# Optimization experiments

Measured on AMD Instinct MI355X. Metric: run time of the kernel, lower is better.

Reference implementation:

```python
import jax, jax.numpy as jnp
import numpy as np

N_REQ = 100000
N_CODE = 100000
C_IN = 256
C_OUT = 256
HEADS = 8
DIM = C_OUT // HEADS  # 32
E = 500000
E_LAB = 200000
NEG_SLOPE = 0.2
BN_EPS = 1e-5


def setup_inputs() -> dict:
    key = jax.random.key(0)
    ks = jax.random.split(key, 20)
    s = 0.05
    return {
        "x_req": jax.random.normal(ks[0], (N_REQ, C_IN), jnp.float32),
        "x_code": jax.random.normal(ks[1], (N_CODE, C_IN), jnp.float32),
        "edge_index_rc": jax.random.randint(ks[2], (2, E), 0, N_CODE),  # req -> code
        "edge_index_cr": jax.random.randint(ks[3], (2, E), 0, N_REQ),   # code -> req
        "edge_label_index": jax.random.randint(ks[4], (2, E_LAB), 0, N_REQ),
        # per-node-type projections
        "W_req": jax.random.normal(ks[5], (C_OUT, C_IN), jnp.float32) * s,
        "b_req": jnp.zeros((C_OUT,), jnp.float32),
        "W_code": jax.random.normal(ks[6], (C_OUT, C_IN), jnp.float32) * s,
        "b_code": jnp.zeros((C_OUT,), jnp.float32),
        # per-edge-type attention vectors [heads, dim]
        "att_src_rc": jax.random.normal(ks[7], (HEADS, DIM), jnp.float32) * s,
        "att_dst_rc": jax.random.normal(ks[8], (HEADS, DIM), jnp.float32) * s,
        "att_src_cr": jax.random.normal(ks[9], (HEADS, DIM), jnp.float32) * s,
        "att_dst_cr": jax.random.normal(ks[10], (HEADS, DIM), jnp.float32) * s,
        # semantic-level attention
        "k_W": jax.random.normal(ks[11], (C_OUT, C_OUT), jnp.float32) * s,
        "k_b": jnp.zeros((C_OUT,), jnp.float32),
        "q": jax.random.normal(ks[12], (C_OUT,), jnp.float32) * s,
        # BatchNorm1d affine params (shared bn1 applied to each node type)
        "gamma": jnp.ones((C_OUT,), jnp.float32),
        "beta": jnp.zeros((C_OUT,), jnp.float32),
    }


def _segment_softmax(logits, seg, num_segments):
    # logits: [E, H], softmax over edges sharing the same destination node
    m = jax.ops.segment_max(logits, seg, num_segments=num_segments)
    m = jnp.where(jnp.isfinite(m), m, 0.0)
    e = jnp.exp(logits - m[seg])
    s = jax.ops.segment_sum(e, seg, num_segments=num_segments)
    return e / (s[seg] + 1e-16)


def _han_edge(x_src, x_dst, edge_index, att_s, att_d, n_dst):
    # x_src: [N_src, H, D], x_dst: [N_dst, H, D]
    a_s = jnp.einsum('nhd,hd->nh', x_src, att_s)
    a_d = jnp.einsum('nhd,hd->nh', x_dst, att_d)
    src, dst = edge_index[0], edge_index[1]
    alpha = jax.nn.leaky_relu(a_s[src] + a_d[dst], NEG_SLOPE)   # [E, H]
    alpha = _segment_softmax(alpha, dst, n_dst)
    msg = x_src[src] * alpha[:, :, None]                        # [E, H, D]
    out = jax.ops.segment_sum(msg, dst, num_segments=n_dst)     # [N_dst, H, D]
    return jax.nn.relu(out.reshape(n_dst, HEADS * DIM))


def _group(outs, q, k_W, k_b):
    # semantic-level attention over metapaths (PyG HANConv group)
    stacked = jnp.stack(outs)                                   # [M, N, C]
    k = jnp.tanh(stacked @ k_W.T + k_b).mean(axis=1)            # [M, C]
    attn = jax.nn.softmax((q * k).sum(-1))                      # [M]
    return jnp.einsum('m,mnc->nc', attn, stacked)


def _batchnorm(x, gamma, beta):
    mu = x.mean(axis=0)
    var = x.var(axis=0)  # biased, as torch BN uses for normalization
    return (x - mu) * jax.lax.rsqrt(var + BN_EPS) * gamma + beta


def reference(x_req, x_code, edge_index_rc, edge_index_cr, edge_label_index,
              W_req, b_req, W_code, b_code,
              att_src_rc, att_dst_rc, att_src_cr, att_dst_cr,
              k_W, k_b, q, gamma, beta):
    # node-type projections -> [N, H, D]
    h_req = (x_req @ W_req.T + b_req).reshape(-1, HEADS, DIM)
    h_code = (x_code @ W_code.T + b_code).reshape(-1, HEADS, DIM)

    # per-edge-type GAT-style propagation
    out_code = _han_edge(h_req, h_code, edge_index_rc, att_src_rc, att_dst_rc, N_CODE)
    out_req = _han_edge(h_code, h_req, edge_index_cr, att_src_cr, att_dst_cr, N_REQ)

    # semantic attention fusion (one metapath per node type here)
    z_req = _group([out_req], q, k_W, k_b)
    z_code = _group([out_code], q, k_W, k_b)

    # shared BatchNorm1d applied per node type (training-mode batch stats)
    z_req = _batchnorm(z_req, gamma, beta)
    z_code = _batchnorm(z_code, gamma, beta)

    # edge dot-product classifier
    feat_req = z_req[edge_label_index[0]]
    feat_code = z_code[edge_label_index[1]]
    return jax.nn.sigmoid((feat_req * feat_code).sum(axis=-1))
```

## Files before the change

kernel.cpp:

```cpp
#include <hip/hip_runtime.h>
#include <cstdint>
#include <cstddef>

namespace {

constexpr int kN    = 100000;
constexpr int kNpad = 100096;
constexpr int kE    = 500000;
constexpr int kEL   = 200000;
constexpr int kC    = 256;
constexpr int kH    = 8;
constexpr float kNegSlope = 0.2f;
constexpr float kBnEps    = 1e-5f;

typedef float    f32x4  __attribute__((ext_vector_type(4)));
typedef __bf16   bf16x8 __attribute__((ext_vector_type(8)));
typedef _Float16 h4     __attribute__((ext_vector_type(4)));

__device__ inline unsigned short bf16_rtn(float x) {
  unsigned u = __builtin_bit_cast(unsigned, x);
  unsigned r = (u + 0x7fffu + ((u >> 16) & 1u)) >> 16;
  return (unsigned short)r;
}
__device__ inline float bf16_f(unsigned short h) {
  unsigned u = ((unsigned)h) << 16;
  return __builtin_bit_cast(float, u);
}

__device__ inline void async_copy16(unsigned short* lds, const unsigned short* g) {
  __builtin_amdgcn_global_load_lds(
      (const __attribute__((address_space(1))) unsigned int*)g,
      (__attribute__((address_space(3))) unsigned int*)lds, 16, 0, 0);
}

__global__ void zero_kernel(int* __restrict__ p, int n) {
  const int i = blockIdx.x * 256 + threadIdx.x;
  if (i < n) p[i] = 0;
}

__global__ __launch_bounds__(256) void cvt_kernel(
    const float* __restrict__ in, unsigned short* __restrict__ hi,
    unsigned short* __restrict__ lo, int n4) {
  const int i = blockIdx.x * 256 + threadIdx.x;
  if (i >= n4) return;
  const float4 v = ((const float4*)in)[i];
  const unsigned short h0 = bf16_rtn(v.x), h1 = bf16_rtn(v.y),
                       h2 = bf16_rtn(v.z), h3 = bf16_rtn(v.w);
  ((ushort4*)hi)[i] = make_ushort4(h0, h1, h2, h3);
  ((ushort4*)lo)[i] = make_ushort4(bf16_rtn(v.x - bf16_f(h0)),
                                   bf16_rtn(v.y - bf16_f(h1)),
                                   bf16_rtn(v.z - bf16_f(h2)),
                                   bf16_rtn(v.w - bf16_f(h3)));
}

__global__ __launch_bounds__(256) void gemm_kernel(
    const unsigned short* __restrict__ Ahi, const unsigned short* __restrict__ Alo,
    const unsigned short* __restrict__ Bhi, const unsigned short* __restrict__ Blo,
    const float* __restrict__ bias, _Float16* __restrict__ H, int M) {
  __shared__ unsigned short sAhi[128 * 32];
  __shared__ unsigned short sAlo[128 * 32];
  __shared__ unsigned short sBhi[128 * 32];
  __shared__ unsigned short sBlo[128 * 32];

  const int tid  = threadIdx.x;
  const int m0   = blockIdx.y * 128;
  const int n0   = blockIdx.x * 128;
  const int w    = tid >> 6, lane = tid & 63, l16 = lane & 15, quad = lane >> 4;
  const int wm   = (w >> 1) * 64, wn = (w & 1) * 64;

  const unsigned short* gsrc = (w == 0) ? Ahi : (w == 1) ? Alo : (w == 2) ? Bhi : Blo;
  unsigned short* lds        = (w == 0) ? sAhi : (w == 1) ? sAlo : (w == 2) ? sBhi : sBlo;
  const int row0 = (w < 2) ? m0 : n0;
  const size_t gbase = (size_t)(row0 + (lane >> 2)) * kC + (lane & 3) * 8;

  f32x4 acc[4][4] = {};

  for (int kt = 0; kt < kC / 32; ++kt) {
    const int k0 = kt * 32;
    __syncthreads();
#pragma unroll
    for (int j = 0; j < 8; ++j)
      async_copy16(lds + j * 512, gsrc + gbase + (size_t)j * 16 * kC + k0);
    __syncthreads();

    bf16x8 ah[4], al[4], bh[4], bl[4];
#pragma unroll
    for (int mi = 0; mi < 4; ++mi) {
      const int row = wm + mi * 16 + l16;
      ah[mi] = *(const bf16x8*)&sAhi[row * 32 + quad * 8];
      al[mi] = *(const bf16x8*)&sAlo[row * 32 + quad * 8];
    }
#pragma unroll
    for (int ni = 0; ni < 4; ++ni) {
      const int row = wn + ni * 16 + l16;
      bh[ni] = *(const bf16x8*)&sBhi[row * 32 + quad * 8];
      bl[ni] = *(const bf16x8*)&sBlo[row * 32 + quad * 8];
    }
#pragma unroll
    for (int mi = 0; mi < 4; ++mi)
#pragma unroll
      for (int ni = 0; ni < 4; ++ni) {
        acc[mi][ni] = __builtin_amdgcn_mfma_f32_16x16x32_bf16(ah[mi], bh[ni], acc[mi][ni], 0, 0, 0);
        acc[mi][ni] = __builtin_amdgcn_mfma_f32_16x16x32_bf16(ah[mi], bl[ni], acc[mi][ni], 0, 0, 0);
        acc[mi][ni] = __builtin_amdgcn_mfma_f32_16x16x32_bf16(al[mi], bh[ni], acc[mi][ni], 0, 0, 0);
      }
  }

#pragma unroll
  for (int ni = 0; ni < 4; ++ni) {
    const int col = n0 + wn + ni * 16 + l16;
    const float bc = bias[col];
#pragma unroll
    for (int mi = 0; mi < 4; ++mi) {
      const int gm0 = m0 + wm + mi * 16 + quad * 4;
#pragma unroll
      for (int r = 0; r < 4; ++r) {
        const int gm = gm0 + r;
        if (gm < M) H[(size_t)gm * kC + col] = (_Float16)(acc[mi][ni][r] + bc);
      }
    }
  }
}

__global__ __launch_bounds__(256) void avec_kernel(
    const _Float16* __restrict__ h, const float* __restrict__ attA,
    const float* __restrict__ attB, float* __restrict__ outA,
    float* __restrict__ outB, int N) {
  const int n = blockIdx.x * 4 + (threadIdx.x >> 6);
  if (n >= N) return;
  const int L = threadIdx.x & 63;
  const h4 hv = *(const h4*)&h[(size_t)n * kC + 4 * L];
  const float4 a = *(const float4*)&attA[4 * L];
  const float4 b = *(const float4*)&attB[4 * L];
  const float hx = (float)hv.x, hy = (float)hv.y, hz = (float)hv.z, hw = (float)hv.w;
  float pa = hx * a.x + hy * a.y + hz * a.z + hw * a.w;
  float pb = hx * b.x + hy * b.y + hz * b.z + hw * b.w;
  for (int m = 1; m < 8; m <<= 1) {
    pa += __shfl_xor(pa, m);
    pb += __shfl_xor(pb, m);
  }
  if ((L & 7) == 0) {
    outA[n * kH + (L >> 3)] = pa;
    outB[n * kH + (L >> 3)] = pb;
  }
}

__global__ void count_kernel(const int* __restrict__ dst, int E, int* __restrict__ cnt) {
  const int e = blockIdx.x * 256 + threadIdx.x;
  if (e < E) atomicAdd(&cnt[dst[e]], 1);
}

__global__ void scan1_kernel(const int* __restrict__ cnt, int N,
                             int* __restrict__ off, int* __restrict__ part) {
  __shared__ int s[256];
  const int t = threadIdx.x;
  const int i = blockIdx.x * 256 + t;
  const int v = (i < N) ? cnt[i] : 0;
  s[t] = v;
  __syncthreads();
  for (int o = 1; o < 256; o <<= 1) {
    const int x = (t >= o) ? s[t - o] : 0;
    __syncthreads();
    s[t] += x;
    __syncthreads();
  }
  if (i < N) off[i] = s[t] - v;
  if (t == 255) part[blockIdx.x] = s[255];
}

__global__ void scan2_kernel(int* __restrict__ part, int NB) {
  __shared__ int s[512];
  const int t = threadIdx.x;
  const int v = (t < NB) ? part[t] : 0;
  s[t] = v;
  __syncthreads();
  for (int o = 1; o < 512; o <<= 1) {
    const int x = (t >= o) ? s[t - o] : 0;
    __syncthreads();
    s[t] += x;
    __syncthreads();
  }
  if (t < NB) part[t] = s[t] - v;
}

__global__ void scan3_kernel(int* __restrict__ off, int* __restrict__ cur,
                             const int* __restrict__ part, int N) {
  const int i = blockIdx.x * 256 + threadIdx.x;
  if (i < N) {
    const int v = off[i] + part[blockIdx.x];
    off[i] = v;
    cur[i] = v;
  }
}

__global__ void scatter_kernel(const int* __restrict__ dst,
                               const int* __restrict__ srcv, int E,
                               int* __restrict__ cur, int* __restrict__ perm) {
  const int e = blockIdx.x * 256 + threadIdx.x;
  if (e < E) {
    const int p = atomicAdd(&cur[dst[e]], 1);
    perm[p] = srcv[e];
  }
}

__global__ __launch_bounds__(256) void aggregate2_kernel(
    const _Float16* __restrict__ h0, const float* __restrict__ aS0,
    const float* __restrict__ aD0, const int* __restrict__ srcs0,
    const int* __restrict__ off0, const int* __restrict__ cnt0,
    float* __restrict__ out0,
    const _Float16* __restrict__ h1, const float* __restrict__ aS1,
    const float* __restrict__ aD1, const int* __restrict__ srcs1,
    const int* __restrict__ off1, const int* __restrict__ cnt1,
    float* __restrict__ out1) {
  const int d = blockIdx.x * 4 + (threadIdx.x >> 6);
  if (d >= kN) return;
  const bool dir1 = (blockIdx.y != 0);
  const _Float16* __restrict__ hsrc = dir1 ? h1 : h0;
  const float* __restrict__ aS   = dir1 ? aS1 : aS0;
  const float* __restrict__ aD   = dir1 ? aD1 : aD0;
  const int* __restrict__ srcs   = dir1 ? srcs1 : srcs0;
  const int* __restrict__ off    = dir1 ? off1 : off0;
  const int* __restrict__ cnt    = dir1 ? cnt1 : cnt0;
  float* __restrict__ out        = dir1 ? out1 : out0;

  const int L  = threadIdx.x & 63;
  const int hd = L >> 3;
  const float ad = aD[d * kH + hd];
  const int o = off[d], c = cnt[d];
  float4 acc = make_float4(0.f, 0.f, 0.f, 0.f);
  float se = 0.f;
  int i = 0;
  for (; i + 4 <= c; i += 4) {
    const int s0 = srcs[o + i], s1 = srcs[o + i + 1];
    const int s2 = srcs[o + i + 2], s3 = srcs[o + i + 3];
    const float a0 = aS[s0 * kH + hd], a1 = aS[s1 * kH + hd];
    const float a2 = aS[s2 * kH + hd], a3 = aS[s3 * kH + hd];
    const h4 v0 = *(const h4*)&hsrc[(size_t)s0 * kC + 4 * L];
    const h4 v1 = *(const h4*)&hsrc[(size_t)s1 * kC + 4 * L];
    const h4 v2 = *(const h4*)&hsrc[(size_t)s2 * kC + 4 * L];
    const h4 v3 = *(const h4*)&hsrc[(size_t)s3 * kC + 4 * L];
    float t0 = a0 + ad; t0 = t0 > 0.f ? t0 : kNegSlope * t0;
    float t1 = a1 + ad; t1 = t1 > 0.f ? t1 : kNegSlope * t1;
    float t2 = a2 + ad; t2 = t2 > 0.f ? t2 : kNegSlope * t2;
    float t3 = a3 + ad; t3 = t3 > 0.f ? t3 : kNegSlope * t3;
    const float w0 = __expf(t0), w1 = __expf(t1);
    const float w2 = __expf(t2), w3 = __expf(t3);
    se += (w0 + w1) + (w2 + w3);
    acc.x += w0 * (float)v0.x + w1 * (float)v1.x + w2 * (float)v2.x + w3 * (float)v3.x;
    acc.y += w0 * (float)v0.y + w1 * (float)v1.y + w2 * (float)v2.y + w3 * (float)v3.y;
    acc.z += w0 * (float)v0.z + w1 * (float)v1.z + w2 * (float)v2.z + w3 * (float)v3.z;
    acc.w += w0 * (float)v0.w + w1 * (float)v1.w + w2 * (float)v2.w + w3 * (float)v3.w;
  }
  for (; i < c; ++i) {
    const int s = srcs[o + i];
    float t = aS[s * kH + hd] + ad;
    t = t > 0.f ? t : kNegSlope * t;
    const float wgt = __expf(t);
    se += wgt;
    const h4 hv = *(const h4*)&hsrc[(size_t)s * kC + 4 * L];
    acc.x += wgt * (float)hv.x;
    acc.y += wgt * (float)hv.y;
    acc.z += wgt * (float)hv.z;
    acc.w += wgt * (float)hv.w;
  }
  const float inv = 1.f / (se + 1e-16f);
  float4 r;
  r.x = fmaxf(acc.x * inv, 0.f);
  r.y = fmaxf(acc.y * inv, 0.f);
  r.z = fmaxf(acc.z * inv, 0.f);
  r.w = fmaxf(acc.w * inv, 0.f);
  *(float4*)&out[(size_t)d * kC + 4 * L] = r;
}

constexpr int kBnB = 512;
__global__ __launch_bounds__(256) void bn_stats_kernel(
    const float* __restrict__ xr, const float* __restrict__ xc,
    float* __restrict__ part) {
  __shared__ f32x4 red[2][4][64];
  const float* __restrict__ x = blockIdx.y ? xc : xr;
  const int t = threadIdx.x, w = t >> 6, L = t & 63;
  const int rowsPer = (kN + kBnB - 1) / kBnB;
  const int r0 = blockIdx.x * rowsPer;
  const int r1 = min(r0 + rowsPer, kN);
  f32x4 s0 = {0.f, 0.f, 0.f, 0.f}, q0 = {0.f, 0.f, 0.f, 0.f};
  f32x4 s1 = {0.f, 0.f, 0.f, 0.f}, q1 = {0.f, 0.f, 0.f, 0.f};
  f32x4 s2 = {0.f, 0.f, 0.f, 0.f}, q2 = {0.f, 0.f, 0.f, 0.f};
  f32x4 s3 = {0.f, 0.f, 0.f, 0.f}, q3 = {0.f, 0.f, 0.f, 0.f};
  int r = r0 + w;
  for (; r + 12 < r1; r += 16) {
    const f32x4 v0 = *(const f32x4*)&x[(size_t)(r)      * kC + 4 * L];
    const f32x4 v1 = *(const f32x4*)&x[(size_t)(r + 4)  * kC + 4 * L];
    const f32x4 v2 = *(const f32x4*)&x[(size_t)(r + 8)  * kC + 4 * L];
    const f32x4 v3 = *(const f32x4*)&x[(size_t)(r + 12) * kC + 4 * L];
    s0 += v0; q0 += v0 * v0;
    s1 += v1; q1 += v1 * v1;
    s2 += v2; q2 += v2 * v2;
    s3 += v3; q3 += v3 * v3;
  }
  for (; r < r1; r += 4) {
    const f32x4 v = *(const f32x4*)&x[(size_t)r * kC + 4 * L];
    s0 += v; q0 += v * v;
  }
  const f32x4 s = (s0 + s1) + (s2 + s3);
  const f32x4 q = (q0 + q1) + (q2 + q3);
  red[0][w][L] = s;
  red[1][w][L] = q;
  __syncthreads();
  if (w == 0) {
    const f32x4 ts = red[0][0][L] + red[0][1][L] + red[0][2][L] + red[0][3][L];
    const f32x4 t2 = red[1][0][L] + red[1][1][L] + red[1][2][L] + red[1][3][L];
    float* dst = part + ((size_t)blockIdx.y * kBnB + blockIdx.x) * 512;
    *(f32x4*)&dst[4 * L]       = ts;
    *(f32x4*)&dst[256 + 4 * L] = t2;
  }
}

__global__ __launch_bounds__(256) void bn_final_kernel(
    const float* __restrict__ part, const float* __restrict__ gamma,
    const float* __restrict__ beta, float* __restrict__ sb) {
  const int c = threadIdx.x;
  const int t = blockIdx.x;
  const float* __restrict__ p0 = part + (size_t)t * kBnB * 512;
  float s = 0.f, q = 0.f;
#pragma unroll 4
  for (int b = 0; b < kBnB; ++b) {
    s += p0[b * 512 + c];
    q += p0[b * 512 + 256 + c];
  }
  const float mu  = s * (1.f / kN);
  const float var = q * (1.f / kN) - mu * mu;
  const float sc  = gamma[c] * rsqrtf(var + kBnEps);
  sb[t * 512 + c]       = sc;
  sb[t * 512 + 256 + c] = beta[c] - mu * sc;
}

__global__ __launch_bounds__(256) void classify_kernel(
    const float* __restrict__ zr, const float* __restrict__ zc,
    const int* __restrict__ ei, const int* __restrict__ ej,
    const float* __restrict__ sb, float* __restrict__ y, int EL) {
  const int e = blockIdx.x * 4 + (threadIdx.x >> 6);
  if (e >= EL) return;
  const int L = threadIdx.x & 63;
  const int i = ei[e], j = ej[e];
  const float4 a  = *(const float4*)&zr[(size_t)i * kC + 4 * L];
  const float4 b  = *(const float4*)&zc[(size_t)j * kC + 4 * L];
  const float4 sr = *(const float4*)&sb[4 * L];
  const float4 br = *(const float4*)&sb[256 + 4 * L];
  const float4 sc = *(const float4*)&sb[512 + 4 * L];
  const float4 bc = *(const float4*)&sb[768 + 4 * L];
  float p = (a.x * sr.x + br.x) * (b.x * sc.x + bc.x) +
            (a.y * sr.y + br.y) * (b.y * sc.y + bc.y) +
            (a.z * sr.z + br.z) * (b.z * sc.z + bc.z) +
            (a.w * sr.w + br.w) * (b.w * sc.w + bc.w);
  for (int m = 1; m < 64; m <<= 1) p += __shfl_xor(p, m);
  if (L == 0) y[e] = 1.f / (1.f + __expf(-p));
}

}

extern "C" void kernel_launch(void* const* d_in, const int* in_sizes, int n_in,
                              void* d_out, int out_size, void* d_ws, size_t ws_size,
                              hipStream_t stream) {
  (void)in_sizes; (void)n_in; (void)out_size; (void)ws_size;
  const float* x_req      = (const float*)d_in[0];
  const float* x_code     = (const float*)d_in[1];
  const int*   ei_rc      = (const int*)d_in[2];
  const int*   ei_cr      = (const int*)d_in[3];
  const int*   el         = (const int*)d_in[4];
  const float* W_req      = (const float*)d_in[5];
  const float* b_req      = (const float*)d_in[6];
  const float* W_code     = (const float*)d_in[7];
  const float* b_code     = (const float*)d_in[8];
  const float* att_src_rc = (const float*)d_in[9];
  const float* att_dst_rc = (const float*)d_in[10];
  const float* att_src_cr = (const float*)d_in[11];
  const float* att_dst_cr = (const float*)d_in[12];
  const float* gamma      = (const float*)d_in[16];
  const float* beta       = (const float*)d_in[17];
  float* y = (float*)d_out;

  char* p = (char*)d_ws;
  auto alloc = [&](size_t bytes) {
    char* r = p;
    p += (bytes + 1023) & ~(size_t)1023;
    return r;
  };
  unsigned short* Xhi = (unsigned short*)alloc((size_t)kNpad * kC * 2);
  unsigned short* Xlo = (unsigned short*)alloc((size_t)kNpad * kC * 2);
  float* out_code = (float*)Xhi;
  _Float16* h_req  = (_Float16*)alloc((size_t)kN * kC * 2);
  _Float16* h_code = (_Float16*)alloc((size_t)kN * kC * 2);
  float* out_req   = (float*)alloc((size_t)kN * kC * 4);
  unsigned short* Whi_r = (unsigned short*)alloc((size_t)kC * kC * 2);
  unsigned short* Wlo_r = (unsigned short*)alloc((size_t)kC * kC * 2);
  unsigned short* Whi_c = (unsigned short*)alloc((size_t)kC * kC * 2);
  unsigned short* Wlo_c = (unsigned short*)alloc((size_t)kC * kC * 2);
  float* a_src_rc = (float*)alloc((size_t)kN * kH * 4);
  float* a_dst_rc = (float*)alloc((size_t)kN * kH * 4);
  float* a_src_cr = (float*)alloc((size_t)kN * kH * 4);
  float* a_dst_cr = (float*)alloc((size_t)kN * kH * 4);
  int* cnt_rc  = (int*)alloc((size_t)kN * 4);
  int* off_rc  = (int*)alloc((size_t)kN * 4);
  int* cur_rc  = (int*)alloc((size_t)kN * 4);
  int* perm_rc = (int*)alloc((size_t)kE * 4);
  int* cnt_cr  = (int*)alloc((size_t)kN * 4);
  int* off_cr  = (int*)alloc((size_t)kN * 4);
  int* cur_cr  = (int*)alloc((size_t)kN * 4);
  int* perm_cr = (int*)alloc((size_t)kE * 4);
  int*   part  = (int*)alloc(512 * 4);
  float* bnpart = (float*)a_src_rc;
  float* sb     = (float*)a_src_cr;

  const int nScanB = (kN + 255) / 256;
  const int nX4    = kN * kC / 4;
  const int nW4    = kC * kC / 4;

  zero_kernel<<<nScanB, 256, 0, stream>>>(cnt_rc, kN);
  zero_kernel<<<nScanB, 256, 0, stream>>>(cnt_cr, kN);

  cvt_kernel<<<(nW4 + 255) / 256, 256, 0, stream>>>(W_req, Whi_r, Wlo_r, nW4);
  cvt_kernel<<<(nW4 + 255) / 256, 256, 0, stream>>>(W_code, Whi_c, Wlo_c, nW4);

  dim3 ggrid(kC / 128, kNpad / 128);
  cvt_kernel<<<(nX4 + 255) / 256, 256, 0, stream>>>(x_req, Xhi, Xlo, nX4);
  gemm_kernel<<<ggrid, 256, 0, stream>>>(Xhi, Xlo, Whi_r, Wlo_r, b_req, h_req, kN);
  cvt_kernel<<<(nX4 + 255) / 256, 256, 0, stream>>>(x_code, Xhi, Xlo, nX4);
  gemm_kernel<<<ggrid, 256, 0, stream>>>(Xhi, Xlo, Whi_c, Wlo_c, b_code, h_code, kN);

  avec_kernel<<<(kN + 3) / 4, 256, 0, stream>>>(h_req, att_src_rc, att_dst_cr,
                                                a_src_rc, a_dst_cr, kN);
  avec_kernel<<<(kN + 3) / 4, 256, 0, stream>>>(h_code, att_src_cr, att_dst_rc,
                                                a_src_cr, a_dst_rc, kN);

  const int* src_rc = ei_rc;
  const int* dst_rc = ei_rc + kE;
  const int* src_cr = ei_cr;
  const int* dst_cr = ei_cr + kE;
  count_kernel<<<(kE + 255) / 256, 256, 0, stream>>>(dst_rc, kE, cnt_rc);
  count_kernel<<<(kE + 255) / 256, 256, 0, stream>>>(dst_cr, kE, cnt_cr);
  scan1_kernel<<<nScanB, 256, 0, stream>>>(cnt_rc, kN, off_rc, part);
  scan2_kernel<<<1, 512, 0, stream>>>(part, nScanB);
  scan3_kernel<<<nScanB, 256, 0, stream>>>(off_rc, cur_rc, part, kN);
  scan1_kernel<<<nScanB, 256, 0, stream>>>(cnt_cr, kN, off_cr, part);
  scan2_kernel<<<1, 512, 0, stream>>>(part, nScanB);
  scan3_kernel<<<nScanB, 256, 0, stream>>>(off_cr, cur_cr, part, kN);
  scatter_kernel<<<(kE + 255) / 256, 256, 0, stream>>>(dst_rc, src_rc, kE, cur_rc, perm_rc);
  scatter_kernel<<<(kE + 255) / 256, 256, 0, stream>>>(dst_cr, src_cr, kE, cur_cr, perm_cr);

  aggregate2_kernel<<<dim3((kN + 3) / 4, 2), 256, 0, stream>>>(
      h_req, a_src_rc, a_dst_rc, perm_rc, off_rc, cnt_rc, out_code,
      h_code, a_src_cr, a_dst_cr, perm_cr, off_cr, cnt_cr, out_req);

  bn_stats_kernel<<<dim3(kBnB, 2), 256, 0, stream>>>(out_req, out_code, bnpart);
  bn_final_kernel<<<2, 256, 0, stream>>>(bnpart, gamma, beta, sb);

  classify_kernel<<<(kEL + 3) / 4, 256, 0, stream>>>(
      out_req, out_code, el, el + kEL, sb, y, kEL);
}
```

Baseline: 825.3 us.

## Fuse fp32-to-bf16 hi/lo split into GEMM and batch both projections

After: 752.2 us. -8.9%, faster.

```diff
diff --git a/kernel.cpp b/kernel.cpp
--- a/kernel.cpp
+++ b/kernel.cpp
@@ -33,9 +33,12 @@
       (__attribute__((address_space(3))) unsigned int*)lds, 16, 0, 0);
 }
 
-__global__ void zero_kernel(int* __restrict__ p, int n) {
+__global__ void zero2_kernel(int* __restrict__ p0, int* __restrict__ p1, int n) {
   const int i = blockIdx.x * 256 + threadIdx.x;
-  if (i < n) p[i] = 0;
+  if (i < n) {
+    p0[i] = 0;
+    p1[i] = 0;
+  }
 }
 
 __global__ __launch_bounds__(256) void cvt_kernel(
@@ -53,14 +56,23 @@
                                    bf16_rtn(v.w - bf16_f(h3)));
 }
 
-__global__ __launch_bounds__(256) void gemm_kernel(
-    const unsigned short* __restrict__ Ahi, const unsigned short* __restrict__ Alo,
-    const unsigned short* __restrict__ Bhi, const unsigned short* __restrict__ Blo,
-    const float* __restrict__ bias, _Float16* __restrict__ H, int M) {
+__global__ __launch_bounds__(256) void gemm_fused_kernel(
+    const float* __restrict__ X0, const float* __restrict__ X1,
+    const unsigned short* __restrict__ Whi0, const unsigned short* __restrict__ Wlo0,
+    const unsigned short* __restrict__ Whi1, const unsigned short* __restrict__ Wlo1,
+    const float* __restrict__ bias0, const float* __restrict__ bias1,
+    _Float16* __restrict__ H0, _Float16* __restrict__ H1) {
   __shared__ unsigned short sAhi[128 * 32];
   __shared__ unsigned short sAlo[128 * 32];
   __shared__ unsigned short sBhi[128 * 32];
   __shared__ unsigned short sBlo[128 * 32];
+
+  const bool t1 = (blockIdx.z != 0);
+  const float* __restrict__ X            = t1 ? X1 : X0;
+  const unsigned short* __restrict__ Whi = t1 ? Whi1 : Whi0;
+  const unsigned short* __restrict__ Wlo = t1 ? Wlo1 : Wlo0;
+  const float* __restrict__ bias         = t1 ? bias1 : bias0;
+  _Float16* __restrict__ H               = t1 ? H1 : H0;
 
   const int tid  = threadIdx.x;
   const int m0   = blockIdx.y * 128;
@@ -68,19 +80,36 @@
   const int w    = tid >> 6, lane = tid & 63, l16 = lane & 15, quad = lane >> 4;
   const int wm   = (w >> 1) * 64, wn = (w & 1) * 64;
 
-  const unsigned short* gsrc = (w == 0) ? Ahi : (w == 1) ? Alo : (w == 2) ? Bhi : Blo;
-  unsigned short* lds        = (w == 0) ? sAhi : (w == 1) ? sAlo : (w == 2) ? sBhi : sBlo;
-  const int row0 = (w < 2) ? m0 : n0;
-  const size_t gbase = (size_t)(row0 + (lane >> 2)) * kC + (lane & 3) * 8;
+  const int arow = w * 32 + (lane >> 3);
+  const int acol = (lane & 7) * 4;
+  const size_t bbase = (size_t)(n0 + (lane >> 2)) * kC + (lane & 3) * 8;
 
   f32x4 acc[4][4] = {};
 
   for (int kt = 0; kt < kC / 32; ++kt) {
     const int k0 = kt * 32;
     __syncthreads();
-#pragma unroll
-    for (int j = 0; j < 8; ++j)
-      async_copy16(lds + j * 512, gsrc + gbase + (size_t)j * 16 * kC + k0);
+    async_copy16(sBhi + (2 * w) * 512,     Whi + bbase + (size_t)(2 * w) * 16 * kC + k0);
+    async_copy16(sBhi + (2 * w + 1) * 512, Whi + bbase + (size_t)(2 * w + 1) * 16 * kC + k0);
+    async_copy16(sBlo + (2 * w) * 512,     Wlo + bbase + (size_t)(2 * w) * 16 * kC + k0);
+    async_copy16(sBlo + (2 * w + 1) * 512, Wlo + bbase + (size_t)(2 * w + 1) * 16 * kC + k0);
+    f32x4 av[4];
+#pragma unroll
+    for (int j = 0; j < 4; ++j) {
+      const int grow = min(m0 + arow + j * 8, kN - 1);
+      av[j] = *(const f32x4*)&X[(size_t)grow * kC + k0 + acol];
+    }
+#pragma unroll
+    for (int j = 0; j < 4; ++j) {
+      const int row = arow + j * 8;
+      ushort4 hi, lo;
+      hi.x = bf16_rtn(av[j][0]); lo.x = bf16_rtn(av[j][0] - bf16_f(hi.x));
+      hi.y = bf16_rtn(av[j][1]); lo.y = bf16_rtn(av[j][1] - bf16_f(hi.y));
+      hi.z = bf16_rtn(av[j][2]); lo.z = bf16_rtn(av[j][2] - bf16_f(hi.z));
+      hi.w = bf16_rtn(av[j][3]); lo.w = bf16_rtn(av[j][3] - bf16_f(hi.w));
+      *(ushort4*)&sAhi[row * 32 + acol] = hi;
+      *(ushort4*)&sAlo[row * 32 + acol] = lo;
+    }
     __syncthreads();
 
     bf16x8 ah[4], al[4], bh[4], bl[4];
@@ -116,7 +145,7 @@
 #pragma unroll
       for (int r = 0; r < 4; ++r) {
         const int gm = gm0 + r;
-        if (gm < M) H[(size_t)gm * kC + col] = (_Float16)(acc[mi][ni][r] + bc);
+        if (gm < kN) H[(size_t)gm * kC + col] = (_Float16)(acc[mi][ni][r] + bc);
       }
     }
   }
@@ -387,6 +416,7 @@
   };
   unsigned short* Xhi = (unsigned short*)alloc((size_t)kNpad * kC * 2);
   unsigned short* Xlo = (unsigned short*)alloc((size_t)kNpad * kC * 2);
+  (void)Xlo;
   float* out_code = (float*)Xhi;
   _Float16* h_req  = (_Float16*)alloc((size_t)kN * kC * 2);
   _Float16* h_code = (_Float16*)alloc((size_t)kN * kC * 2);
@@ -412,20 +442,15 @@
   float* sb     = (float*)a_src_cr;
 
   const int nScanB = (kN + 255) / 256;
-  const int nX4    = kN * kC / 4;
   const int nW4    = kC * kC / 4;
 
-  zero_kernel<<<nScanB, 256, 0, stream>>>(cnt_rc, kN);
-  zero_kernel<<<nScanB, 256, 0, stream>>>(cnt_cr, kN);
+  zero2_kernel<<<nScanB, 256, 0, stream>>>(cnt_rc, cnt_cr, kN);
 
   cvt_kernel<<<(nW4 + 255) / 256, 256, 0, stream>>>(W_req, Whi_r, Wlo_r, nW4);
   cvt_kernel<<<(nW4 + 255) / 256, 256, 0, stream>>>(W_code, Whi_c, Wlo_c, nW4);
 
-  dim3 ggrid(kC / 128, kNpad / 128);
-  cvt_kernel<<<(nX4 + 255) / 256, 256, 0, stream>>>(x_req, Xhi, Xlo, nX4);
-  gemm_kernel<<<ggrid, 256, 0, stream>>>(Xhi, Xlo, Whi_r, Wlo_r, b_req, h_req, kN);
-  cvt_kernel<<<(nX4 + 255) / 256, 256, 0, stream>>>(x_code, Xhi, Xlo, nX4);
-  gemm_kernel<<<ggrid, 256, 0, stream>>>(Xhi, Xlo, Whi_c, Wlo_c, b_code, h_code, kN);
+  gemm_fused_kernel<<<dim3(kC / 128, kNpad / 128, 2), 256, 0, stream>>>(
+      x_req, x_code, Whi_r, Wlo_r, Whi_c, Wlo_c, b_req, b_code, h_req, h_code);
 
   avec_kernel<<<(kN + 3) / 4, 256, 0, stream>>>(h_req, att_src_rc, att_dst_cr,
                                                 a_src_rc, a_dst_cr, kN);
```
